# Kernel optimization log

Hardware: AMD Instinct MI355X
Metric: run time of the kernel (lower is better)

The kernel has to match this reference:

```python
import jax, jax.numpy as jnp
import numpy as np

NUM_HEADS = 12
TEMPORAL_RES = 8


def _ln(x, g, b, eps=1e-5):
    mu = jnp.mean(x, axis=-1, keepdims=True)
    var = jnp.mean((x - mu) ** 2, axis=-1, keepdims=True)
    return (x - mu) * jax.lax.rsqrt(var + eps) * g + b


def setup_inputs() -> dict:
    key = jax.random.key(0)
    ks = jax.random.split(key, 8)
    s = 0.02
    d = 768
    inp = {
        'box_tensors': jax.random.uniform(ks[0], (16, 16, 10, 4), dtype=jnp.float32),
        'box_categories': jax.random.normal(ks[1], (16, 10, d), dtype=jnp.float32) * s,
        'w1': jax.random.normal(ks[2], (4, d // 2), dtype=jnp.float32) * s,
        'w2': jax.random.normal(ks[3], (d // 2, d), dtype=jnp.float32) * s,
        'ln1_g': jnp.ones((d,), jnp.float32),
        'ln1_b': jnp.zeros((d,), jnp.float32),
        'wqkv': jax.random.normal(ks[4], (d, 3 * d), dtype=jnp.float32) * s,
        'wo': jax.random.normal(ks[5], (d, d), dtype=jnp.float32) * s,
        'bo': jnp.zeros((d,), jnp.float32),
        'ln2_g': jnp.ones((d,), jnp.float32),
        'ln2_b': jnp.zeros((d,), jnp.float32),
        'wfc1': jax.random.normal(ks[6], (d, 4 * d), dtype=jnp.float32) * s,
        'bfc1': jnp.zeros((4 * d,), jnp.float32),
        'wfc2': jax.random.normal(ks[7], (4 * d, d), dtype=jnp.float32) * s,
        'bfc2': jnp.zeros((d,), jnp.float32),
        'H': 14,
        'W': 14,
    }
    return inp


def _forward(box_tensors, box_categories, w1, w2, ln1_g, ln1_b, wqkv, wo, bo,
             ln2_g, ln2_b, wfc1, bfc1, wfc2, bfc2, H, W):
    B, T, O, _ = box_tensors.shape
    d = box_categories.shape[-1]
    # coord -> feature MLP (no biases), then pos-emb add
    h = jax.nn.relu(box_tensors @ w1)
    x = jax.nn.relu(h @ w2)                      # [B,T,O,d]
    x = x + box_categories[None]                 # broadcast over batch
    L = T * O
    x = x.reshape(B, L, d)
    # --- self-attention block (pre-LN ViT style) ---
    hn = _ln(x, ln1_g, ln1_b)
    qkv = (hn @ wqkv).reshape(B, L, 3, NUM_HEADS, d // NUM_HEADS)
    q, k, v = qkv[:, :, 0], qkv[:, :, 1], qkv[:, :, 2]   # [B,L,h,dh]
    scale = 1.0 / jnp.sqrt(jnp.asarray(d // NUM_HEADS, x.dtype))
    att = jnp.einsum('bqhd,bkhd->bhqk', q, k) * scale
    att = jax.nn.softmax(att, axis=-1)
    o = jnp.einsum('bhqk,bkhd->bqhd', att, v).reshape(B, L, d)
    x = x + (o @ wo + bo)
    hn = _ln(x, ln2_g, ln2_b)
    x = x + (jax.nn.gelu(hn @ wfc1 + bfc1, approximate=False) @ wfc2 + bfc2)
    feats = x.reshape(B, T, O, d)
    # --- box2spatial layout scatter: sum each object's feature into grid cells inside its box ---
    x1 = jnp.minimum(box_tensors[..., 0], box_tensors[..., 2])
    x2 = jnp.maximum(box_tensors[..., 0], box_tensors[..., 2])
    y1 = jnp.minimum(box_tensors[..., 1], box_tensors[..., 3])
    y2 = jnp.maximum(box_tensors[..., 1], box_tensors[..., 3])
    cy = (jnp.arange(H, dtype=x.dtype) + 0.5) / H    # [H]
    cx = (jnp.arange(W, dtype=x.dtype) + 0.5) / W    # [W]
    in_y = (cy[None, None, None, :] >= y1[..., None]) & (cy[None, None, None, :] <= y2[..., None])  # [B,T,O,H]
    in_x = (cx[None, None, None, :] >= x1[..., None]) & (cx[None, None, None, :] <= x2[..., None])  # [B,T,O,W]
    mask = (in_y[..., :, None] & in_x[..., None, :]).astype(x.dtype)  # [B,T,O,H,W]
    grid = jnp.einsum('btohw,btod->bthwd', mask, feats)               # [B,T,H,W,d]
    # temporal avg pooling to TEMPORAL_RES frames
    Tr = T // TEMPORAL_RES
    if Tr > 1:
        grid = grid.reshape(B, T // Tr, Tr, H, W, d).mean(axis=2)
    return grid.reshape(B, -1, d)                 # [B, T'*H*W, d]


def reference(box_tensors, box_categories, w1, w2, ln1_g, ln1_b, wqkv, wo, bo,
              ln2_g, ln2_b, wfc1, bfc1, wfc2, bfc2, H, W):
    return _forward(box_tensors, box_categories, w1, w2, ln1_g, ln1_b, wqkv, wo, bo,
                    ln2_g, ln2_b, wfc1, bfc1, wfc2, bfc2, H, W)
```

## Files before the change

kernel.cpp:

```cpp
#include <hip/hip_runtime.h>
#include <hip/hip_bf16.h>
#include <math.h>


#define BATCH 16
#define TT    16
#define OO    10
#define LL    160
#define BL    2560
#define DD    768
#define NH    12
#define DH    64
#define GH    14
#define GW    14
#define TGRP  8

typedef unsigned short ushort_t;
typedef __attribute__((ext_vector_type(8))) __bf16 bf16x8;
typedef __attribute__((ext_vector_type(4))) float f32x4;

__device__ __forceinline__ ushort_t f2bf(float f) {
    unsigned int u = __float_as_uint(f);
    u += 0x7fffu + ((u >> 16) & 1u);
    return (ushort_t)(u >> 16);
}

__global__ __launch_bounds__(256)
void transpose_w(const float* __restrict__ W, ushort_t* __restrict__ Wt, int K, int N)
{
    __shared__ float s[32][33];
    const int n0 = blockIdx.x * 32, k0 = blockIdx.y * 32;
    const int tx = threadIdx.x & 31, ty = threadIdx.x >> 5;
#pragma unroll
    for (int r = 0; r < 4; ++r)
        s[ty + r * 8][tx] = W[(size_t)(k0 + ty + r * 8) * N + n0 + tx];
    __syncthreads();
#pragma unroll
    for (int r = 0; r < 4; ++r)
        Wt[(size_t)(n0 + ty + r * 8) * K + k0 + tx] = f2bf(s[tx][ty + r * 8]);
}

__global__ __launch_bounds__(256)
void box_h(const float* __restrict__ box, const float* __restrict__ w1,
           ushort_t* __restrict__ h)
{
    const int idx = blockIdx.x * 256 + threadIdx.x;
    const int r = idx / 384, j = idx - r * 384;
    const float* bx = box + (size_t)r * 4;
    float v = bx[0] * w1[j] + bx[1] * w1[384 + j] +
              bx[2] * w1[768 + j] + bx[3] * w1[1152 + j];
    h[idx] = f2bf(fmaxf(v, 0.f));
}

__global__ __launch_bounds__(256)
void ln_kernel(const float* __restrict__ in, const float* __restrict__ g,
               const float* __restrict__ bvec, ushort_t* __restrict__ out)
{
    const int r = blockIdx.x;
    const int tid = threadIdx.x;
    const float* row = in + (size_t)r * DD;
    float v0 = row[tid], v1 = row[tid + 256], v2 = row[tid + 512];
    float s  = v0 + v1 + v2;
    float s2 = v0 * v0 + v1 * v1 + v2 * v2;
#pragma unroll
    for (int off = 32; off > 0; off >>= 1) {
        s  += __shfl_down(s, off);
        s2 += __shfl_down(s2, off);
    }
    __shared__ float red[8];
    int wave = tid >> 6, lane = tid & 63;
    if (lane == 0) { red[wave] = s; red[wave + 4] = s2; }
    __syncthreads();
    s  = red[0] + red[1] + red[2] + red[3];
    s2 = red[4] + red[5] + red[6] + red[7];
    float mu  = s * (1.f / DD);
    float var = s2 * (1.f / DD) - mu * mu;
    float inv = rsqrtf(var + 1e-5f);
    ushort_t* op = out + (size_t)r * DD;
    op[tid]       = f2bf((v0 - mu) * inv * g[tid]       + bvec[tid]);
    op[tid + 256] = f2bf((v1 - mu) * inv * g[tid + 256] + bvec[tid + 256]);
    op[tid + 512] = f2bf((v2 - mu) * inv * g[tid + 512] + bvec[tid + 512]);
}

#define LOADF(aa, bb, kk)                                                        \
    _Pragma("unroll")                                                            \
    for (int i = 0; i < 4; ++i) {                                                \
        aa[i] = *reinterpret_cast<const bf16x8*>(ap + (size_t)(i * 16) * lda + (kk)); \
        bb[i] = *reinterpret_cast<const bf16x8*>(bp + (size_t)(i * 16) * ldb + (kk)); \
    }
#define MFMA16(aa, bb)                                                           \
    _Pragma("unroll")                                                            \
    for (int i = 0; i < 4; ++i)                                                  \
        _Pragma("unroll")                                                        \
        for (int j = 0; j < 4; ++j)                                              \
            acc[i][j] = __builtin_amdgcn_mfma_f32_16x16x32_bf16(aa[i], bb[j], acc[i][j], 0, 0, 0);

template <int MODE, int SPLIT>
__global__ __launch_bounds__(64)
void gemm_rf(const ushort_t* __restrict__ A, int lda,
             const ushort_t* __restrict__ Bt, int ldb,
             const float* __restrict__ bias, const float* __restrict__ cat,
             float* __restrict__ Cf, ushort_t* __restrict__ Cb,
             int ldc, int K)
{
    const int lane = threadIdx.x;
    const int l16 = lane & 15, quad = lane >> 4;
    const int row0 = blockIdx.y * 64, col0 = blockIdx.x * 64;
    const int Kper = K / SPLIT;
    const int k0 = blockIdx.z * Kper;

    const ushort_t* ap = A  + (size_t)(row0 + l16) * lda + k0 + quad * 8;
    const ushort_t* bp = Bt + (size_t)(col0 + l16) * ldb + k0 + quad * 8;

    f32x4 acc[4][4];
#pragma unroll
    for (int i = 0; i < 4; ++i)
#pragma unroll
        for (int j = 0; j < 4; ++j) {
            acc[i][j][0] = 0.f; acc[i][j][1] = 0.f;
            acc[i][j][2] = 0.f; acc[i][j][3] = 0.f;
        }

    bf16x8 a0[4], b0[4], a1[4], b1[4];
    LOADF(a0, b0, 0)
    int kt = 0;
    for (; kt + 64 < Kper; kt += 64) {
        LOADF(a1, b1, kt + 32)
        MFMA16(a0, b0)
        LOADF(a0, b0, kt + 64)
        MFMA16(a1, b1)
    }
    LOADF(a1, b1, kt + 32)
    MFMA16(a0, b0)
    MFMA16(a1, b1)

    const int q4 = quad * 4;
#pragma unroll
    for (int i = 0; i < 4; ++i)
#pragma unroll
        for (int j = 0; j < 4; ++j) {
            const int gcol = col0 + j * 16 + l16;
            const float bj = (MODE == 1 || MODE == 2)
                               ? ((SPLIT == 1 || blockIdx.z == 0) ? bias[gcol] : 0.f)
                               : 0.f;
#pragma unroll
            for (int r = 0; r < 4; ++r) {
                const int grow = row0 + i * 16 + q4 + r;
                const size_t idx = (size_t)grow * ldc + gcol;
                const float v = acc[i][j][r];
                if (MODE == 1) {
                    if (SPLIT > 1) atomicAdd(&Cf[idx], v + bj);
                    else           Cf[idx] += v + bj;
                } else if (MODE == 2) {
                    const float u = v + bj;
                    Cb[idx] = f2bf(0.5f * u * (1.f + erff(u * 0.70710678118654752f)));
                } else if (MODE == 3) {
                    Cb[idx] = f2bf(v);
                } else {
                    Cf[idx] = fmaxf(v, 0.f) + cat[(size_t)(grow % LL) * DD + gcol];
                }
            }
        }
}

#define GLL(gp, lp) __builtin_amdgcn_global_load_lds(                       \
    (const __attribute__((address_space(1))) void*)(gp),                     \
    (__attribute__((address_space(3))) void*)(lp), 16, 0, 0)

template <int MODE, int SPLIT>
__global__ __launch_bounds__(256)
void gemm_lds(const ushort_t* __restrict__ A, int lda,
              const ushort_t* __restrict__ Bt, int ldb,
              const float* __restrict__ bias,
              float* __restrict__ Cf, ushort_t* __restrict__ Cb,
              int ldc, int K)
{
    __shared__ ushort_t As[2][4096];
    __shared__ ushort_t Bs[2][4096];

    const int t    = threadIdx.x;
    const int wv   = t >> 6;
    const int lane = t & 63;
    const int l16  = lane & 15, quad = lane >> 4;
    const int wr   = (wv >> 1) * 64;
    const int wc   = (wv & 1) * 64;

    const int row0 = blockIdx.y * 128, col0 = blockIdx.x * 128;
    const int Kper = K / SPLIT;
    const int k0   = blockIdx.z * Kper;
    const int steps = Kper / 32;

    const int srow  = t & 127;
    const int skq0  = t >> 7;
    const ushort_t* Ag = A  + (size_t)(row0 + srow) * lda + k0 + skq0 * 8;
    const ushort_t* Bg = Bt + (size_t)(col0 + srow) * ldb + k0 + skq0 * 8;

#define STAGE(c, kk) do {                                                    \
        GLL(Ag + (kk),      &As[c][wv * 512]);                               \
        GLL(Ag + (kk) + 16, &As[c][2048 + wv * 512]);                        \
        GLL(Bg + (kk),      &Bs[c][wv * 512]);                               \
        GLL(Bg + (kk) + 16, &Bs[c][2048 + wv * 512]);                        \
    } while (0)

    f32x4 acc[4][4];
#pragma unroll
    for (int i = 0; i < 4; ++i)
#pragma unroll
        for (int j = 0; j < 4; ++j) {
            acc[i][j][0] = 0.f; acc[i][j][1] = 0.f;
            acc[i][j][2] = 0.f; acc[i][j][3] = 0.f;
        }

    STAGE(0, 0);
    __syncthreads();
    int cur = 0;
    for (int s = 0; s < steps; ++s) {
        if (s + 1 < steps) STAGE(cur ^ 1, (s + 1) * 32);
        bf16x8 af[4], bfr[4];
#pragma unroll
        for (int i = 0; i < 4; ++i)
            af[i] = *reinterpret_cast<const bf16x8*>(
                &As[cur][quad * 1024 + (wr + i * 16 + l16) * 8]);
#pragma unroll
        for (int j = 0; j < 4; ++j)
            bfr[j] = *reinterpret_cast<const bf16x8*>(
                &Bs[cur][quad * 1024 + (wc + j * 16 + l16) * 8]);
#pragma unroll
        for (int i = 0; i < 4; ++i)
#pragma unroll
            for (int j = 0; j < 4; ++j)
                acc[i][j] = __builtin_amdgcn_mfma_f32_16x16x32_bf16(
                    af[i], bfr[j], acc[i][j], 0, 0, 0);
        __syncthreads();
        cur ^= 1;
    }
#undef STAGE

    const int q4 = quad * 4;
    const int r0w = row0 + wr, c0w = col0 + wc;
#pragma unroll
    for (int i = 0; i < 4; ++i)
#pragma unroll
        for (int j = 0; j < 4; ++j) {
            const int gcol = c0w + j * 16 + l16;
            const float bj = (MODE == 1 || MODE == 2)
                               ? ((SPLIT == 1 || blockIdx.z == 0) ? bias[gcol] : 0.f)
                               : 0.f;
#pragma unroll
            for (int r = 0; r < 4; ++r) {
                const int grow = r0w + i * 16 + q4 + r;
                const size_t idx = (size_t)grow * ldc + gcol;
                const float v = acc[i][j][r];
                if (MODE == 1) {
                    if (SPLIT > 1) atomicAdd(&Cf[idx], v + bj);
                    else           Cf[idx] += v + bj;
                } else if (MODE == 2) {
                    const float u = v + bj;
                    Cb[idx] = f2bf(0.5f * u * (1.f + erff(u * 0.70710678118654752f)));
                } else {
                    Cb[idx] = f2bf(v);
                }
            }
        }
}

#define KS_STRIDE 72
#define VT_STRIDE 168
__global__ __launch_bounds__(320)
void attention_mfma(ushort_t* __restrict__ qkv)
{
    __shared__ ushort_t Ks[160 * KS_STRIDE];
    __shared__ ushort_t Vt[64 * VT_STRIDE];
    __shared__ ushort_t Pb[5][32 * VT_STRIDE];

    const int b  = blockIdx.x / NH;
    const int hh = blockIdx.x % NH;
    ushort_t* basew = qkv + (size_t)b * LL * (3 * DD) + hh * DH;
    const ushort_t* base = basew;
    const int tid  = threadIdx.x;
    const int wave = tid >> 6, lane = tid & 63;
    const int l16 = lane & 15, quad = lane >> 4;

#pragma unroll
    for (int it = 0; it < 4; ++it) {
        int idx = tid + it * 320;
        int l = idx >> 3, c8 = (idx & 7) * 8;
        uint4 kv = *(const uint4*)(base + (size_t)l * (3 * DD) + DD + c8);
        *(uint4*)&Ks[l * KS_STRIDE + c8] = kv;
        uint4 vv = *(const uint4*)(base + (size_t)l * (3 * DD) + 2 * DD + c8);
        ushort_t e[8];
        *(uint4*)e = vv;
#pragma unroll
        for (int i = 0; i < 8; ++i)
            Vt[(c8 + i) * VT_STRIDE + l] = e[i];
    }

    const int q0 = wave * 32;
    bf16x8 qf[2][2];
#pragma unroll
    for (int t = 0; t < 2; ++t)
#pragma unroll
        for (int k = 0; k < 2; ++k)
            qf[t][k] = *reinterpret_cast<const bf16x8*>(
                base + (size_t)(q0 + t * 16 + l16) * (3 * DD) + k * 32 + quad * 8);

    __syncthreads();

    f32x4 S0[10], S1[10];
#pragma unroll
    for (int nt = 0; nt < 10; ++nt) {
        f32x4 z = {0.f, 0.f, 0.f, 0.f};
        const ushort_t* kb = &Ks[(nt * 16 + l16) * KS_STRIDE + quad * 8];
        bf16x8 kf0 = *reinterpret_cast<const bf16x8*>(kb);
        bf16x8 kf1 = *reinterpret_cast<const bf16x8*>(kb + 32);
        f32x4 a0 = __builtin_amdgcn_mfma_f32_16x16x32_bf16(qf[0][0], kf0, z, 0, 0, 0);
        S0[nt]   = __builtin_amdgcn_mfma_f32_16x16x32_bf16(qf[0][1], kf1, a0, 0, 0, 0);
        f32x4 a1 = __builtin_amdgcn_mfma_f32_16x16x32_bf16(qf[1][0], kf0, z, 0, 0, 0);
        S1[nt]   = __builtin_amdgcn_mfma_f32_16x16x32_bf16(qf[1][1], kf1, a1, 0, 0, 0);
    }

#pragma unroll
    for (int t = 0; t < 2; ++t) {
        f32x4* S = t ? S1 : S0;
        float mrow[4] = {-1e30f, -1e30f, -1e30f, -1e30f};
#pragma unroll
        for (int nt = 0; nt < 10; ++nt)
#pragma unroll
            for (int r = 0; r < 4; ++r) {
                S[nt][r] *= 0.125f;
                mrow[r] = fmaxf(mrow[r], S[nt][r]);
            }
#pragma unroll
        for (int r = 0; r < 4; ++r) {
            mrow[r] = fmaxf(mrow[r], __shfl_xor(mrow[r], 1));
            mrow[r] = fmaxf(mrow[r], __shfl_xor(mrow[r], 2));
            mrow[r] = fmaxf(mrow[r], __shfl_xor(mrow[r], 4));
            mrow[r] = fmaxf(mrow[r], __shfl_xor(mrow[r], 8));
        }
        float lsum[4] = {0.f, 0.f, 0.f, 0.f};
#pragma unroll
        for (int nt = 0; nt < 10; ++nt)
#pragma unroll
            for (int r = 0; r < 4; ++r) {
                float e = __expf(S[nt][r] - mrow[r]);
                S[nt][r] = e;
                lsum[r] += e;
            }
#pragma unroll
        for (int r = 0; r < 4; ++r) {
            lsum[r] += __shfl_xor(lsum[r], 1);
            lsum[r] += __shfl_xor(lsum[r], 2);
            lsum[r] += __shfl_xor(lsum[r], 4);
            lsum[r] += __shfl_xor(lsum[r], 8);
            lsum[r] = 1.f / lsum[r];
        }
#pragma unroll
        for (int nt = 0; nt < 10; ++nt)
#pragma unroll
            for (int r = 0; r < 4; ++r)
                Pb[wave][(t * 16 + quad * 4 + r) * VT_STRIDE + nt * 16 + l16] =
                    f2bf(S[nt][r] * lsum[r]);
    }
    asm volatile("s_waitcnt lgkmcnt(0)" ::: "memory");

#pragma unroll
    for (int dt = 0; dt < 4; ++dt) {
        f32x4 o0 = {0.f, 0.f, 0.f, 0.f}, o1 = {0.f, 0.f, 0.f, 0.f};
#pragma unroll
        for (int ks = 0; ks < 5; ++ks) {
            bf16x8 vf = *reinterpret_cast<const bf16x8*>(
                &Vt[(dt * 16 + l16) * VT_STRIDE + ks * 32 + quad * 8]);
            bf16x8 p0 = *reinterpret_cast<const bf16x8*>(
                &Pb[wave][(l16) * VT_STRIDE + ks * 32 + quad * 8]);
            bf16x8 p1 = *reinterpret_cast<const bf16x8*>(
                &Pb[wave][(16 + l16) * VT_STRIDE + ks * 32 + quad * 8]);
            o0 = __builtin_amdgcn_mfma_f32_16x16x32_bf16(vf, p0, o0, 0, 0, 0);
            o1 = __builtin_amdgcn_mfma_f32_16x16x32_bf16(vf, p1, o1, 0, 0, 0);
        }
#pragma unroll
        for (int t = 0; t < 2; ++t) {
            f32x4 o = t ? o1 : o0;
            ushort_t pk[4];
#pragma unroll
            for (int r = 0; r < 4; ++r) pk[r] = f2bf(o[r]);
            ushort_t* dst = basew + (size_t)(q0 + t * 16 + l16) * (3 * DD) +
                            dt * 16 + quad * 4;
            *(uint2*)dst = *(const uint2*)pk;
        }
    }
}

__global__ __launch_bounds__(256)
void mask_grid(const float* __restrict__ box, const float* __restrict__ feats,
               float* __restrict__ out)
{
    const int hw = blockIdx.x;
    const int g  = blockIdx.y;
    const int b  = blockIdx.z;
    const int hh = hw / GW, w = hw % GW;
    const float cy = (hh + 0.5f) / (float)GH;
    const float cx = (w  + 0.5f) / (float)GW;
    const int tid = threadIdx.x;

    __shared__ float flg[20];
    if (tid < 20) {
        int t = g * 2 + tid / OO, o = tid % OO;
        const float* bx = box + (size_t)((b * TT + t) * OO + o) * 4;
        float x1 = fminf(bx[0], bx[2]), x2 = fmaxf(bx[0], bx[2]);
        float y1 = fminf(bx[1], bx[3]), y2 = fmaxf(bx[1], bx[3]);
        flg[tid] = (cy >= y1 && cy <= y2 && cx >= x1 && cx <= x2) ? 1.f : 0.f;
    }
    __syncthreads();

    float a0 = 0.f, a1 = 0.f, a2 = 0.f;
#pragma unroll
    for (int p = 0; p < 20; ++p) {
        if (flg[p] != 0.f) {
            int r = (b * TT + g * 2 + p / OO) * OO + (p % OO);
            const float* f = feats + (size_t)r * DD;
            a0 += f[tid]; a1 += f[tid + 256]; a2 += f[tid + 512];
        }
    }
    float* op = out + ((size_t)b * (TGRP * GH * GW) + g * (GH * GW) + hw) * DD;
    op[tid]       = a0 * 0.5f;
    op[tid + 256] = a1 * 0.5f;
    op[tid + 512] = a2 * 0.5f;
}

extern "C" void kernel_launch(void* const* d_in, const int* in_sizes, int n_in,
                              void* d_out, int out_size, void* d_ws, size_t ws_size,
                              hipStream_t stream)
{
    const float* box  = (const float*)d_in[0];
    const float* cat  = (const float*)d_in[1];
    const float* w1   = (const float*)d_in[2];
    const float* w2   = (const float*)d_in[3];
    const float* ln1g = (const float*)d_in[4];
    const float* ln1b = (const float*)d_in[5];
    const float* wqkv = (const float*)d_in[6];
    const float* wo   = (const float*)d_in[7];
    const float* bo   = (const float*)d_in[8];
    const float* ln2g = (const float*)d_in[9];
    const float* ln2b = (const float*)d_in[10];
    const float* wfc1 = (const float*)d_in[11];
    const float* bfc1 = (const float*)d_in[12];
    const float* wfc2 = (const float*)d_in[13];
    const float* bfc2 = (const float*)d_in[14];
    float* out = (float*)d_out;

    char* wsb = (char*)d_ws;
    float*    x     = (float*)   (wsb + 0);
    ushort_t* qkvb  = (ushort_t*)(wsb + 7864320);
    ushort_t* fc1b  = qkvb;
    ushort_t* hnb   = (ushort_t*)(wsb + 23592960);
    ushort_t* wqkvT = (ushort_t*)(wsb + 27525120);
    ushort_t* woT   = (ushort_t*)(wsb + 31064064);
    ushort_t* wfc1T = (ushort_t*)(wsb + 32243712);
    ushort_t* wfc2T = (ushort_t*)(wsb + 36962304);
    ushort_t* w2T   = (ushort_t*)(wsb + 41680896);
    ushort_t* h     = (ushort_t*)(wsb + 42270720);

    transpose_w<<<dim3(2304 / 32, 768 / 32), 256, 0, stream>>>(wqkv, wqkvT, 768, 2304);
    transpose_w<<<dim3(768 / 32, 768 / 32), 256, 0, stream>>>(wo, woT, 768, 768);
    transpose_w<<<dim3(3072 / 32, 768 / 32), 256, 0, stream>>>(wfc1, wfc1T, 768, 3072);
    transpose_w<<<dim3(768 / 32, 3072 / 32), 256, 0, stream>>>(wfc2, wfc2T, 3072, 768);
    transpose_w<<<dim3(768 / 32, 384 / 32), 256, 0, stream>>>(w2, w2T, 384, 768);

    box_h<<<BL * 384 / 256, 256, 0, stream>>>(box, w1, h);
    gemm_rf<4, 1><<<dim3(12, 40, 1), 64, 0, stream>>>(h, 384, w2T, 384, nullptr, cat,
                                                      x, nullptr, DD, 384);
    ln_kernel<<<BL, 256, 0, stream>>>(x, ln1g, ln1b, hnb);
    gemm_lds<3, 1><<<dim3(2304 / 128, 2560 / 128, 1), 256, 0, stream>>>(
        hnb, DD, wqkvT, DD, nullptr, nullptr, qkvb, 3 * DD, DD);
    attention_mfma<<<BATCH * NH, 320, 0, stream>>>(qkvb);
    gemm_lds<1, 2><<<dim3(768 / 128, 2560 / 128, 2), 256, 0, stream>>>(
        qkvb, 3 * DD, woT, DD, bo, x, nullptr, DD, DD);
    ln_kernel<<<BL, 256, 0, stream>>>(x, ln2g, ln2b, hnb);
    gemm_lds<2, 1><<<dim3(3072 / 128, 2560 / 128, 1), 256, 0, stream>>>(
        hnb, DD, wfc1T, DD, bfc1, nullptr, fc1b, 4 * DD, DD);
    gemm_lds<1, 4><<<dim3(768 / 128, 2560 / 128, 4), 256, 0, stream>>>(
        fc1b, 4 * DD, wfc2T, 4 * DD, bfc2, x, nullptr, DD, 4 * DD);
    mask_grid<<<dim3(GH * GW, TGRP, BATCH), 256, 0, stream>>>(box, x, out);
}
```

Baseline: 334.0 us.

## Deepen GEMM LDS pipeline to four stages and replace split-K with 128x64 tiles

The LDS GEMM moves from a double buffer with __syncthreads to a four-buffer ring with three stages in flight, using explicit vmcnt waits and raw barriers. The split-K launches for the output projection and FC2 are replaced by a 128x64 tile variant with no split, which removes the float atomics and gives a plain read-modify-write epilogue. The register-file GEMM is stripped down to its single used mode. The deeper ring uses more LDS and may lower occupancy, and the hand-tuned vmcnt counts must match the number of loads issued per stage.

After: 359.2 us. 1.08x slower.

```diff
diff --git a/kernel.cpp b/kernel.cpp
--- a/kernel.cpp
+++ b/kernel.cpp
@@ -95,22 +95,18 @@
         for (int j = 0; j < 4; ++j)                                              \
             acc[i][j] = __builtin_amdgcn_mfma_f32_16x16x32_bf16(aa[i], bb[j], acc[i][j], 0, 0, 0);
 
-template <int MODE, int SPLIT>
 __global__ __launch_bounds__(64)
 void gemm_rf(const ushort_t* __restrict__ A, int lda,
              const ushort_t* __restrict__ Bt, int ldb,
-             const float* __restrict__ bias, const float* __restrict__ cat,
-             float* __restrict__ Cf, ushort_t* __restrict__ Cb,
-             int ldc, int K)
+             const float* __restrict__ cat,
+             float* __restrict__ Cf, int ldc, int K)
 {
     const int lane = threadIdx.x;
     const int l16 = lane & 15, quad = lane >> 4;
     const int row0 = blockIdx.y * 64, col0 = blockIdx.x * 64;
-    const int Kper = K / SPLIT;
-    const int k0 = blockIdx.z * Kper;
-
-    const ushort_t* ap = A  + (size_t)(row0 + l16) * lda + k0 + quad * 8;
-    const ushort_t* bp = Bt + (size_t)(col0 + l16) * ldb + k0 + quad * 8;
+
+    const ushort_t* ap = A  + (size_t)(row0 + l16) * lda + quad * 8;
+    const ushort_t* bp = Bt + (size_t)(col0 + l16) * ldb + quad * 8;
 
     f32x4 acc[4][4];
 #pragma unroll
@@ -124,7 +120,7 @@
     bf16x8 a0[4], b0[4], a1[4], b1[4];
     LOADF(a0, b0, 0)
     int kt = 0;
-    for (; kt + 64 < Kper; kt += 64) {
+    for (; kt + 64 < K; kt += 64) {
         LOADF(a1, b1, kt + 32)
         MFMA16(a0, b0)
         LOADF(a0, b0, kt + 64)
@@ -140,25 +136,11 @@
 #pragma unroll
         for (int j = 0; j < 4; ++j) {
             const int gcol = col0 + j * 16 + l16;
-            const float bj = (MODE == 1 || MODE == 2)
-                               ? ((SPLIT == 1 || blockIdx.z == 0) ? bias[gcol] : 0.f)
-                               : 0.f;
 #pragma unroll
             for (int r = 0; r < 4; ++r) {
                 const int grow = row0 + i * 16 + q4 + r;
                 const size_t idx = (size_t)grow * ldc + gcol;
-                const float v = acc[i][j][r];
-                if (MODE == 1) {
-                    if (SPLIT > 1) atomicAdd(&Cf[idx], v + bj);
-                    else           Cf[idx] += v + bj;
-                } else if (MODE == 2) {
-                    const float u = v + bj;
-                    Cb[idx] = f2bf(0.5f * u * (1.f + erff(u * 0.70710678118654752f)));
-                } else if (MODE == 3) {
-                    Cb[idx] = f2bf(v);
-                } else {
-                    Cf[idx] = fmaxf(v, 0.f) + cat[(size_t)(grow % LL) * DD + gcol];
-                }
+                Cf[idx] = fmaxf(acc[i][j][r], 0.f) + cat[(size_t)(grow % LL) * DD + gcol];
             }
         }
 }
@@ -167,7 +149,9 @@
     (const __attribute__((address_space(1))) void*)(gp),                     \
     (__attribute__((address_space(3))) void*)(lp), 16, 0, 0)
 
-template <int MODE, int SPLIT>
+#define WAITV(n) asm volatile("s_waitcnt vmcnt(" #n ")" ::: "memory")
+
+template <int MODE, int BN>
 __global__ __launch_bounds__(256)
 void gemm_lds(const ushort_t* __restrict__ A, int lda,
               const ushort_t* __restrict__ Bt, int ldb,
@@ -175,36 +159,41 @@
               float* __restrict__ Cf, ushort_t* __restrict__ Cb,
               int ldc, int K)
 {
-    __shared__ ushort_t As[2][4096];
-    __shared__ ushort_t Bs[2][4096];
+    constexpr int NB = 4;
+    constexpr int MI = (BN == 128) ? 4 : 2;
+    constexpr int G  = (BN == 128) ? 4 : 3;
+    __shared__ ushort_t As[NB][4096];
+    __shared__ ushort_t Bs[NB][BN * 32];
 
     const int t    = threadIdx.x;
     const int wv   = t >> 6;
     const int lane = t & 63;
     const int l16  = lane & 15, quad = lane >> 4;
-    const int wr   = (wv >> 1) * 64;
-    const int wc   = (wv & 1) * 64;
-
-    const int row0 = blockIdx.y * 128, col0 = blockIdx.x * 128;
-    const int Kper = K / SPLIT;
-    const int k0   = blockIdx.z * Kper;
-    const int steps = Kper / 32;
-
-    const int srow  = t & 127;
-    const int skq0  = t >> 7;
-    const ushort_t* Ag = A  + (size_t)(row0 + srow) * lda + k0 + skq0 * 8;
-    const ushort_t* Bg = Bt + (size_t)(col0 + srow) * ldb + k0 + skq0 * 8;
+    const int wr   = (BN == 128) ? (wv >> 1) * 64 : wv * 32;
+    const int wc   = (BN == 128) ? (wv & 1) * 64 : 0;
+
+    const int row0 = blockIdx.y * 128, col0 = blockIdx.x * BN;
+    const int steps = K / 32;
+
+    const ushort_t* Ag = A + (size_t)(row0 + (t & 127)) * lda + ((t >> 7) * 8);
+    const int brow = (BN == 128) ? (t & 127) : (t & 63);
+    const int bkq8 = (BN == 128) ? ((t >> 7) * 8) : (wv * 8);
+    const ushort_t* Bg = Bt + (size_t)(col0 + brow) * ldb + bkq8;
 
 #define STAGE(c, kk) do {                                                    \
         GLL(Ag + (kk),      &As[c][wv * 512]);                               \
         GLL(Ag + (kk) + 16, &As[c][2048 + wv * 512]);                        \
-        GLL(Bg + (kk),      &Bs[c][wv * 512]);                               \
-        GLL(Bg + (kk) + 16, &Bs[c][2048 + wv * 512]);                        \
+        if constexpr (BN == 128) {                                           \
+            GLL(Bg + (kk),      &Bs[c][wv * 512]);                           \
+            GLL(Bg + (kk) + 16, &Bs[c][2048 + wv * 512]);                    \
+        } else {                                                             \
+            GLL(Bg + (kk),      &Bs[c][wv * 512]);                           \
+        }                                                                    \
     } while (0)
 
-    f32x4 acc[4][4];
-#pragma unroll
-    for (int i = 0; i < 4; ++i)
+    f32x4 acc[MI][4];
+#pragma unroll
+    for (int i = 0; i < MI; ++i)
 #pragma unroll
         for (int j = 0; j < 4; ++j) {
             acc[i][j][0] = 0.f; acc[i][j][1] = 0.f;
@@ -212,48 +201,56 @@
         }
 
     STAGE(0, 0);
-    __syncthreads();
-    int cur = 0;
+    STAGE(1, 32);
+    STAGE(2, 64);
+
     for (int s = 0; s < steps; ++s) {
-        if (s + 1 < steps) STAGE(cur ^ 1, (s + 1) * 32);
-        bf16x8 af[4], bfr[4];
-#pragma unroll
-        for (int i = 0; i < 4; ++i)
+        const int ah = steps - 1 - s;
+        if (ah >= 2)      { if constexpr (G == 4) WAITV(8); else WAITV(6); }
+        else if (ah == 1) { if constexpr (G == 4) WAITV(4); else WAITV(3); }
+        else              WAITV(0);
+        __builtin_amdgcn_s_barrier();
+        __builtin_amdgcn_sched_barrier(0);
+
+        if (s + 3 < steps) STAGE((s + 3) & 3, (s + 3) * 32);
+
+        const int cur = s & 3;
+        bf16x8 af[MI], bfr[4];
+#pragma unroll
+        for (int i = 0; i < MI; ++i)
             af[i] = *reinterpret_cast<const bf16x8*>(
                 &As[cur][quad * 1024 + (wr + i * 16 + l16) * 8]);
 #pragma unroll
         for (int j = 0; j < 4; ++j)
             bfr[j] = *reinterpret_cast<const bf16x8*>(
-                &Bs[cur][quad * 1024 + (wc + j * 16 + l16) * 8]);
-#pragma unroll
-        for (int i = 0; i < 4; ++i)
+                &Bs[cur][quad * (BN * 8) + (wc + j * 16 + l16) * 8]);
+        asm volatile("s_waitcnt lgkmcnt(0)" ::: "memory");
+        __builtin_amdgcn_sched_barrier(0);
+
+#pragma unroll
+        for (int i = 0; i < MI; ++i)
 #pragma unroll
             for (int j = 0; j < 4; ++j)
                 acc[i][j] = __builtin_amdgcn_mfma_f32_16x16x32_bf16(
                     af[i], bfr[j], acc[i][j], 0, 0, 0);
-        __syncthreads();
-        cur ^= 1;
     }
 #undef STAGE
 
     const int q4 = quad * 4;
     const int r0w = row0 + wr, c0w = col0 + wc;
 #pragma unroll
-    for (int i = 0; i < 4; ++i)
+    for (int i = 0; i < MI; ++i)
 #pragma unroll
         for (int j = 0; j < 4; ++j) {
             const int gcol = c0w + j * 16 + l16;
-            const float bj = (MODE == 1 || MODE == 2)
-                               ? ((SPLIT == 1 || blockIdx.z == 0) ? bias[gcol] : 0.f)
-                               : 0.f;
+            const float bj = (MODE == 1 || MODE == 2) ? bias[gcol] : 0.f;
 #pragma unroll
             for (int r = 0; r < 4; ++r) {
                 const int grow = r0w + i * 16 + q4 + r;
                 const size_t idx = (size_t)grow * ldc + gcol;
                 const float v = acc[i][j][r];
                 if (MODE == 1) {
-                    if (SPLIT > 1) atomicAdd(&Cf[idx], v + bj);
-                    else           Cf[idx] += v + bj;
+                    Cf[idx] += v + bj;
                 } else if (MODE == 2) {
                     const float u = v + bj;
                     Cb[idx] = f2bf(0.5f * u * (1.f + erff(u * 0.70710678118654752f)));
@@ -467,18 +464,17 @@
     transpose_w<<<dim3(768 / 32, 384 / 32), 256, 0, stream>>>(w2, w2T, 384, 768);
 
     box_h<<<BL * 384 / 256, 256, 0, stream>>>(box, w1, h);
-    gemm_rf<4, 1><<<dim3(12, 40, 1), 64, 0, stream>>>(h, 384, w2T, 384, nullptr, cat,
-                                                      x, nullptr, DD, 384);
+    gemm_rf<<<dim3(12, 40, 1), 64, 0, stream>>>(h, 384, w2T, 384, cat, x, DD, 384);
     ln_kernel<<<BL, 256, 0, stream>>>(x, ln1g, ln1b, hnb);
-    gemm_lds<3, 1><<<dim3(2304 / 128, 2560 / 128, 1), 256, 0, stream>>>(
+    gemm_lds<3, 128><<<dim3(2304 / 128, 2560 / 128, 1), 256, 0, stream>>>(
         hnb, DD, wqkvT, DD, nullptr, nullptr, qkvb, 3 * DD, DD);
     attention_mfma<<<BATCH * NH, 320, 0, stream>>>(qkvb);
-    gemm_lds<1, 2><<<dim3(768 / 128, 2560 / 128, 2), 256, 0, stream>>>(
+    gemm_lds<1, 64><<<dim3(768 / 64, 2560 / 128, 1), 256, 0, stream>>>(
         qkvb, 3 * DD, woT, DD, bo, x, nullptr, DD, DD);
     ln_kernel<<<BL, 256, 0, stream>>>(x, ln2g, ln2b, hnb);
-    gemm_lds<2, 1><<<dim3(3072 / 128, 2560 / 128, 1), 256, 0, stream>>>(
+    gemm_lds<2, 128><<<dim3(3072 / 128, 2560 / 128, 1), 256, 0, stream>>>(
         hnb, DD, wfc1T, DD, bfc1, nullptr, fc1b, 4 * DD, DD);
-    gemm_lds<1, 4><<<dim3(768 / 128, 2560 / 128, 4), 256, 0, stream>>>(
+    gemm_lds<1, 64><<<dim3(768 / 64, 2560 / 128, 1), 256, 0, stream>>>(
         fc1b, 4 * DD, wfc2T, 4 * DD, bfc2, x, nullptr, DD, 4 * DD);
     mask_grid<<<dim3(GH * GW, TGRP, BATCH), 256, 0, stream>>>(box, x, out);
 }
```

## Deepen LDS GEMM K-step to 64 and swizzle workgroups across XCDs

Applied to the files above, without the earlier changes.

The LDS GEMM now stages 64 K-elements per buffer instead of 32, doubling shared memory per stage and halving the number of barriers and loop iterations. Workgroup IDs are remapped so consecutive tiles land on the same XCD, to improve L2 reuse of shared A/B panels. The register-file GEMM is de-templated to its single used mode, which is cleanup. The larger LDS footprint (64KB per block) may reduce occupancy.

Result: no change. 334.0 us (+0.0%).

```diff
diff --git a/kernel.cpp b/kernel.cpp
--- a/kernel.cpp
+++ b/kernel.cpp
@@ -23,6 +23,10 @@
     unsigned int u = __float_as_uint(f);
     u += 0x7fffu + ((u >> 16) & 1u);
     return (ushort_t)(u >> 16);
+}
+
+__device__ __forceinline__ int swz_xcd(int bid, int nwg) {
+    return (bid & 7) * (nwg >> 3) + (bid >> 3);
 }
 
 __global__ __launch_bounds__(256)
@@ -95,22 +99,18 @@
         for (int j = 0; j < 4; ++j)                                              \
             acc[i][j] = __builtin_amdgcn_mfma_f32_16x16x32_bf16(aa[i], bb[j], acc[i][j], 0, 0, 0);
 
-template <int MODE, int SPLIT>
 __global__ __launch_bounds__(64)
 void gemm_rf(const ushort_t* __restrict__ A, int lda,
              const ushort_t* __restrict__ Bt, int ldb,
-             const float* __restrict__ bias, const float* __restrict__ cat,
-             float* __restrict__ Cf, ushort_t* __restrict__ Cb,
-             int ldc, int K)
+             const float* __restrict__ cat,
+             float* __restrict__ Cf, int ldc, int K)
 {
     const int lane = threadIdx.x;
     const int l16 = lane & 15, quad = lane >> 4;
     const int row0 = blockIdx.y * 64, col0 = blockIdx.x * 64;
-    const int Kper = K / SPLIT;
-    const int k0 = blockIdx.z * Kper;
-
-    const ushort_t* ap = A  + (size_t)(row0 + l16) * lda + k0 + quad * 8;
-    const ushort_t* bp = Bt + (size_t)(col0 + l16) * ldb + k0 + quad * 8;
+
+    const ushort_t* ap = A  + (size_t)(row0 + l16) * lda + quad * 8;
+    const ushort_t* bp = Bt + (size_t)(col0 + l16) * ldb + quad * 8;
 
     f32x4 acc[4][4];
 #pragma unroll
@@ -124,7 +124,7 @@
     bf16x8 a0[4], b0[4], a1[4], b1[4];
     LOADF(a0, b0, 0)
     int kt = 0;
-    for (; kt + 64 < Kper; kt += 64) {
+    for (; kt + 64 < K; kt += 64) {
         LOADF(a1, b1, kt + 32)
         MFMA16(a0, b0)
         LOADF(a0, b0, kt + 64)
@@ -140,25 +140,11 @@
 #pragma unroll
         for (int j = 0; j < 4; ++j) {
             const int gcol = col0 + j * 16 + l16;
-            const float bj = (MODE == 1 || MODE == 2)
-                               ? ((SPLIT == 1 || blockIdx.z == 0) ? bias[gcol] : 0.f)
-                               : 0.f;
 #pragma unroll
             for (int r = 0; r < 4; ++r) {
                 const int grow = row0 + i * 16 + q4 + r;
                 const size_t idx = (size_t)grow * ldc + gcol;
-                const float v = acc[i][j][r];
-                if (MODE == 1) {
-                    if (SPLIT > 1) atomicAdd(&Cf[idx], v + bj);
-                    else           Cf[idx] += v + bj;
-                } else if (MODE == 2) {
-                    const float u = v + bj;
-                    Cb[idx] = f2bf(0.5f * u * (1.f + erff(u * 0.70710678118654752f)));
-                } else if (MODE == 3) {
-                    Cb[idx] = f2bf(v);
-                } else {
-                    Cf[idx] = fmaxf(v, 0.f) + cat[(size_t)(grow % LL) * DD + gcol];
-                }
+                Cf[idx] = fmaxf(acc[i][j][r], 0.f) + cat[(size_t)(grow % LL) * DD + gcol];
             }
         }
 }
@@ -175,8 +161,8 @@
               float* __restrict__ Cf, ushort_t* __restrict__ Cb,
               int ldc, int K)
 {
-    __shared__ ushort_t As[2][4096];
-    __shared__ ushort_t Bs[2][4096];
+    __shared__ ushort_t As[2][8192];
+    __shared__ ushort_t Bs[2][8192];
 
     const int t    = threadIdx.x;
     const int wv   = t >> 6;
@@ -185,21 +171,28 @@
     const int wr   = (wv >> 1) * 64;
     const int wc   = (wv & 1) * 64;
 
-    const int row0 = blockIdx.y * 128, col0 = blockIdx.x * 128;
+    const int nwg = gridDim.x * gridDim.y * gridDim.z;
+    const int bid = blockIdx.x + gridDim.x * (blockIdx.y + gridDim.y * blockIdx.z);
+    const int w   = swz_xcd(bid, nwg);
+    const int bx  = w % gridDim.x;
+    const int byz = w / gridDim.x;
+    const int by  = byz % gridDim.y;
+    const int bz  = byz / gridDim.y;
+
+    const int row0 = by * 128, col0 = bx * 128;
     const int Kper = K / SPLIT;
-    const int k0   = blockIdx.z * Kper;
-    const int steps = Kper / 32;
-
-    const int srow  = t & 127;
-    const int skq0  = t >> 7;
-    const ushort_t* Ag = A  + (size_t)(row0 + srow) * lda + k0 + skq0 * 8;
-    const ushort_t* Bg = Bt + (size_t)(col0 + srow) * ldb + k0 + skq0 * 8;
+    const int k0   = bz * Kper;
+    const int steps = Kper / 64;
+
+    const ushort_t* Ag = A  + (size_t)(row0 + (t & 127)) * lda + k0 + ((t >> 7) * 8);
+    const ushort_t* Bg = Bt + (size_t)(col0 + (t & 127)) * ldb + k0 + ((t >> 7) * 8);
 
 #define STAGE(c, kk) do {                                                    \
-        GLL(Ag + (kk),      &As[c][wv * 512]);                               \
-        GLL(Ag + (kk) + 16, &As[c][2048 + wv * 512]);                        \
-        GLL(Bg + (kk),      &Bs[c][wv * 512]);                               \
-        GLL(Bg + (kk) + 16, &Bs[c][2048 + wv * 512]);                        \
+        _Pragma("unroll")                                                    \
+        for (int ii = 0; ii < 4; ++ii) {                                     \
+            GLL(Ag + (kk) + ii * 16, &As[c][ii * 2048 + wv * 512]);          \
+            GLL(Bg + (kk) + ii * 16, &Bs[c][ii * 2048 + wv * 512]);          \
+        }                                                                    \
     } while (0)
 
     f32x4 acc[4][4];
@@ -215,22 +208,25 @@
     __syncthreads();
     int cur = 0;
     for (int s = 0; s < steps; ++s) {
-        if (s + 1 < steps) STAGE(cur ^ 1, (s + 1) * 32);
-        bf16x8 af[4], bfr[4];
-#pragma unroll
-        for (int i = 0; i < 4; ++i)
-            af[i] = *reinterpret_cast<const bf16x8*>(
-                &As[cur][quad * 1024 + (wr + i * 16 + l16) * 8]);
-#pragma unroll
-        for (int j = 0; j < 4; ++j)
-            bfr[j] = *reinterpret_cast<const bf16x8*>(
-                &Bs[cur][quad * 1024 + (wc + j * 16 + l16) * 8]);
-#pragma unroll
-        for (int i = 0; i < 4; ++i)
+        if (s + 1 < steps) STAGE(cur ^ 1, (s + 1) * 64);
+#pragma unroll
+        for (int ks = 0; ks < 2; ++ks) {
+            bf16x8 af[4], bfr[4];
+#pragma unroll
+            for (int i = 0; i < 4; ++i)
+                af[i] = *reinterpret_cast<const bf16x8*>(
+                    &As[cur][((ks * 4 + quad) * 128 + wr + i * 16 + l16) * 8]);
 #pragma unroll
             for (int j = 0; j < 4; ++j)
-                acc[i][j] = __builtin_amdgcn_mfma_f32_16x16x32_bf16(
-                    af[i], bfr[j], acc[i][j], 0, 0, 0);
+                bfr[j] = *reinterpret_cast<const bf16x8*>(
+                    &Bs[cur][((ks * 4 + quad) * 128 + wc + j * 16 + l16) * 8]);
+#pragma unroll
+            for (int i = 0; i < 4; ++i)
+#pragma unroll
+                for (int j = 0; j < 4; ++j)
+                    acc[i][j] = __builtin_amdgcn_mfma_f32_16x16x32_bf16(
+                        af[i], bfr[j], acc[i][j], 0, 0, 0);
+        }
         __syncthreads();
         cur ^= 1;
     }
@@ -244,7 +240,7 @@
         for (int j = 0; j < 4; ++j) {
             const int gcol = c0w + j * 16 + l16;
             const float bj = (MODE == 1 || MODE == 2)
-                               ? ((SPLIT == 1 || blockIdx.z == 0) ? bias[gcol] : 0.f)
+                               ? ((SPLIT == 1 || bz == 0) ? bias[gcol] : 0.f)
                                : 0.f;
 #pragma unroll
             for (int r = 0; r < 4; ++r) {
@@ -467,8 +463,7 @@
     transpose_w<<<dim3(768 / 32, 384 / 32), 256, 0, stream>>>(w2, w2T, 384, 768);
 
     box_h<<<BL * 384 / 256, 256, 0, stream>>>(box, w1, h);
-    gemm_rf<4, 1><<<dim3(12, 40, 1), 64, 0, stream>>>(h, 384, w2T, 384, nullptr, cat,
-                                                      x, nullptr, DD, 384);
+    gemm_rf<<<dim3(12, 40, 1), 64, 0, stream>>>(h, 384, w2T, 384, cat, x, DD, 384);
     ln_kernel<<<BL, 256, 0, stream>>>(x, ln1g, ln1b, hnb);
     gemm_lds<3, 1><<<dim3(2304 / 128, 2560 / 128, 1), 256, 0, stream>>>(
         hnb, DD, wqkvT, DD, nullptr, nullptr, qkvb, 3 * DD, DD);
```
